# Kernel optimization log

Measured on AMD Instinct MI355X. Metric: run time of the kernel, lower is better.

The kernel has to match this reference:

```python
import jax, jax.numpy as jnp
import numpy as np

N_NODES = 100000
N_EDGES = 1000000
HEADS = 3
NEG_SLOPE_ATTN = 0.2   # DGL EdgeGATConv default negative_slope
NEG_SLOPE_MLP = 0.01   # torch nn.LeakyReLU default


def _edge_softmax(e, dst, num_nodes):
    # softmax over incoming edges of each destination node; e: [E,H]
    m = jax.ops.segment_max(e, dst, num_segments=num_nodes)
    ex = jnp.exp(e - m[dst])
    s = jax.ops.segment_sum(ex, dst, num_segments=num_nodes)
    return ex / s[dst]


def _edge_gat(h, ef, src, dst, Wfc, Wedge, al, ar, ae, Wres, b, D):
    # Faithful to dgl.nn.EdgeGATConv (residual=True, bias=True defaults).
    N = h.shape[0]
    H = HEADS
    ft = (h @ Wfc).reshape(N, H, D)        # [N,H,D] projected node feats
    fe = (ef @ Wedge).reshape(-1, H, D)    # [E,H,D] projected edge feats
    el = jnp.einsum('nhd,hd->nh', ft, al)
    er = jnp.einsum('nhd,hd->nh', ft, ar)
    ee = jnp.einsum('ehd,hd->eh', fe, ae)
    e = jax.nn.leaky_relu(el[src] + er[dst] + ee, NEG_SLOPE_ATTN)  # [E,H]
    a = _edge_softmax(e, dst, N)                                   # [E,H]
    rst = jax.ops.segment_sum(ft[src] * a[..., None], dst, num_segments=N)
    # residual projection + bias (DGL defaults residual=True, bias=True)
    return rst + (h @ Wres).reshape(N, H, D) + b.reshape(1, H, D)


def _forward(node_feats, edge_feats,
             W1, We1, al1, ar1, ae1, Wr1, b1,
             W2, We2, al2, ar2, ae2, Wr2, b2,
             W3, We3, al3, ar3, ae3, Wr3, b3,
             L1a_w, L1a_b, L1b_w, L1b_b, L1c_w, L1c_b, L2_w, L2_b,
             src, dst):
    h1 = _edge_gat(node_feats, edge_feats, src, dst, W1, We1, al1, ar1, ae1, Wr1, b1, 8)
    h2 = _edge_gat(h1.mean(axis=1), edge_feats, src, dst, W2, We2, al2, ar2, ae2, Wr2, b2, 16)
    h3 = _edge_gat(h2.mean(axis=1), edge_feats, src, dst, W3, We3, al3, ar3, ae3, Wr3, b3, 32)
    # linear1 MLP head applied per (node, head)
    x = jax.nn.leaky_relu(h3 @ L1a_w + L1a_b, NEG_SLOPE_MLP)   # [N,H,16]
    x = jax.nn.leaky_relu(x @ L1b_w + L1b_b, NEG_SLOPE_MLP)    # [N,H,4]
    x = x @ L1c_w + L1c_b                                       # [N,H,1]
    x = x.reshape(x.shape[0], -1) @ L2_w + L2_b                 # [N,1]
    return jnp.max(x, axis=0)                                   # [1]


def setup_inputs() -> dict:
    key = jax.random.key(0)
    ks = iter(jax.random.split(key, 64))

    def nrm(shape, scale=0.1):
        return jax.random.normal(next(ks), shape, dtype=jnp.float32) * scale

    inp = {
        'node_feats': jax.random.normal(next(ks), (N_NODES, 6), dtype=jnp.float32),
        'edge_feats': jax.random.uniform(next(ks), (N_EDGES, 1), dtype=jnp.float32),
    }
    dims = [(6, 8), (8, 16), (16, 32)]
    for i, (din, dout) in enumerate(dims, start=1):
        inp[f'W{i}'] = nrm((din, HEADS * dout))
        inp[f'We{i}'] = nrm((1, HEADS * dout))
        inp[f'al{i}'] = nrm((HEADS, dout))
        inp[f'ar{i}'] = nrm((HEADS, dout))
        inp[f'ae{i}'] = nrm((HEADS, dout))
        inp[f'Wr{i}'] = nrm((din, HEADS * dout))
        inp[f'b{i}'] = nrm((HEADS * dout,))
    inp['L1a_w'] = nrm((32, 16)); inp['L1a_b'] = nrm((16,))
    inp['L1b_w'] = nrm((16, 4));  inp['L1b_b'] = nrm((4,))
    inp['L1c_w'] = nrm((4, 1));   inp['L1c_b'] = nrm((1,))
    inp['L2_w'] = nrm((HEADS, 1)); inp['L2_b'] = nrm((1,))
    inp['src'] = jax.random.randint(next(ks), (N_EDGES,), 0, N_NODES, dtype=jnp.int32)
    inp['dst'] = jax.random.randint(next(ks), (N_EDGES,), 0, N_NODES, dtype=jnp.int32)
    return inp


def reference(node_feats, edge_feats,
              W1, We1, al1, ar1, ae1, Wr1, b1,
              W2, We2, al2, ar2, ae2, Wr2, b2,
              W3, We3, al3, ar3, ae3, Wr3, b3,
              L1a_w, L1a_b, L1b_w, L1b_b, L1c_w, L1c_b, L2_w, L2_b,
              src, dst):
    return _forward(node_feats, edge_feats,
                    W1, We1, al1, ar1, ae1, Wr1, b1,
                    W2, We2, al2, ar2, ae2, Wr2, b2,
                    W3, We3, al3, ar3, ae3, Wr3, b3,
                    L1a_w, L1a_b, L1b_w, L1b_b, L1c_w, L1c_b, L2_w, L2_b,
                    src, dst)
```

## Files before the change

### kernel.cpp

```cpp
#include <hip/hip_runtime.h>
#include <hip/hip_fp16.h>
#include <math.h>

#define NN 100000
#define NE 1000000
#define NCHUNK 160
#define CHUNK (NE/NCHUNK)
#define NODE_RANGE (NN/8)
#define CAPS 24
#define GXS (NCHUNK*8)

typedef unsigned int   u32;
typedef unsigned short u16;

__device__ __forceinline__ float lrelu(float x, float sl){ return x >= 0.f ? x : sl*x; }

__device__ __forceinline__ void atomicMaxF(float* a, float v){
    if (v >= 0.f) atomicMax((int*)a, __float_as_int(v));
    else          atomicMin((unsigned int*)a, __float_as_uint(v));
}

template<int DIN, int DINP, int D, bool WRM>
__device__ void coefBody(const float* __restrict__ Wfc, const float* __restrict__ al,
                         const float* __restrict__ ar, const float* __restrict__ We,
                         const float* __restrict__ ae, const float* __restrict__ Wres,
                         const float* __restrict__ bias,
                         float* __restrict__ q, float* __restrict__ r, float* __restrict__ ce,
                         float* __restrict__ wrm, float* __restrict__ bm){
    int t = threadIdx.x;
    for (int i = t; i < 3*DINP; i += 256){
        int hd = i/DINP, k = i - hd*DINP;
        float qa = 0.f, ra = 0.f;
        if (k < DIN){
            for (int d = 0; d < D; ++d){
                float w = Wfc[k*3*D + hd*D + d];
                qa += w*al[hd*D+d];
                ra += w*ar[hd*D+d];
            }
        }
        q[i] = qa; r[i] = ra;
    }
    if (t < 3){
        float c = 0.f;
        for (int d = 0; d < D; ++d) c += We[t*D+d]*ae[t*D+d];
        ce[t] = c;
    }
    if (WRM){
        for (int i = t; i < DIN*D; i += 256){
            int k = i/D, d = i - k*D;
            wrm[i] = (Wres[k*3*D+d] + Wres[k*3*D+D+d] + Wres[k*3*D+2*D+d])*(1.f/3.f);
        }
        for (int i = t; i < D; i += 256)
            bm[i] = (bias[i] + bias[D+i] + bias[2*D+i])*(1.f/3.f);
    }
}

__global__ void __launch_bounds__(256) kScatPrep(
    const int* __restrict__ src, const int* __restrict__ dst,
    const float* __restrict__ ef,
    int* __restrict__ deg, u32* __restrict__ pack,
    int* __restrict__ ovfc, int4* __restrict__ ovf,
    const float* W1, const float* al1, const float* ar1, const float* We1,
    const float* ae1, const float* Wr1, const float* b1,
    const float* W2, const float* al2, const float* ar2, const float* We2,
    const float* ae2, const float* Wr2, const float* b2,
    const float* W3, const float* al3, const float* ar3, const float* We3,
    const float* ae3, const float* Wr3, const float* b3,
    const float* L1a_w, const float* L1a_b,
    float* coef, float* FA, float* FR, float* C0,
    const float* __restrict__ nf, u32* __restrict__ ntab1, float* __restrict__ er3a,
    float* __restrict__ out)
{
    if (blockIdx.x < GXS){
        const int xcd  = blockIdx.x & 7;
        const int base = (blockIdx.x >> 3)*CHUNK;
        for (int e = base + threadIdx.x; e < base + CHUNK; e += 256){
            int d = __builtin_nontemporal_load(dst + e);
            if (d / NODE_RANGE == xcd){
                int s    = __builtin_nontemporal_load(src + e);
                float fv = __builtin_nontemporal_load(ef + e);
                int pos = atomicAdd(&deg[d], 1);
                if (pos < CAPS){
                    u32 rec = ((u32)s << 15) | (u32)(fv*32767.f + 0.5f);
                    pack[(size_t)d*CAPS + pos] = rec;
                } else {
                    int o = atomicAdd(ovfc, 1);
                    ovf[o] = make_int4(d, s, __float_as_int(fv), 0);
                }
            }
        }
        return;
    }
    const int bid = blockIdx.x - GXS;
    if (bid == 0){
        if (threadIdx.x == 255) out[0] = -INFINITY;
        coefBody<6,8,8,true>(W1, al1, ar1, We1, ae1, Wr1, b1,
            coef+0, coef+24, coef+48, coef+52, coef+100);
    } else if (bid == 1){
        coefBody<8,8,16,true>(W2, al2, ar2, We2, ae2, Wr2, b2,
            coef+108, coef+132, coef+156, coef+160, coef+288);
    } else if (bid == 2){
        coefBody<16,16,32,false>(W3, al3, ar3, We3, ae3, Wr3, b3,
            coef+304, coef+352, coef+400, nullptr, nullptr);
    } else if (bid == 3){
        int t = threadIdx.x;
        for (int i = t; i < 768; i += 256){
            int hd = i >> 8, rem = i & 255;
            int k = rem >> 4, ii = rem & 15;
            float a = 0.f, r = 0.f;
            for (int d = 0; d < 32; ++d){
                float w = L1a_w[d*16 + ii];
                a += W3[k*96 + hd*32 + d]*w;
                r += Wr3[k*96 + hd*32 + d]*w;
            }
            FA[i] = a; FR[i] = r;
        }
        if (t < 48){
            int hd = t >> 4, ii = t & 15;
            float c = L1a_b[ii];
            for (int d = 0; d < 32; ++d) c += b3[hd*32 + d]*L1a_w[d*16 + ii];
            C0[t] = c;
        }
    } else {
        __shared__ float r1s[24];
        int t = threadIdx.x;
        if (t < 24){
            int hd = t >> 3, k = t & 7;
            float ra = 0.f;
            if (k < 6)
                for (int d = 0; d < 8; ++d) ra += W1[k*24 + hd*8 + d]*ar1[hd*8 + d];
            r1s[t] = ra;
        }
        __syncthreads();
        int n = (bid - 4)*256 + t;
        if (n >= NN) return;
        float h[6];
        #pragma unroll
        for (int k = 0; k < 6; ++k) h[k] = nf[(size_t)n*6 + k];
        __half2 p0 = __floats2half2_rn(h[0], h[1]);
        __half2 p1 = __floats2half2_rn(h[2], h[3]);
        __half2 p2 = __floats2half2_rn(h[4], h[5]);
        __half2 p3 = __floats2half2_rn(0.f, 0.f);
        uint4 row;
        row.x = *(u32*)&p0; row.y = *(u32*)&p1; row.z = *(u32*)&p2; row.w = *(u32*)&p3;
        *(uint4*)(ntab1 + (size_t)n*4) = row;
        #pragma unroll
        for (int hd = 0; hd < 3; ++hd){
            float er = 0.f;
            #pragma unroll
            for (int k = 0; k < 6; ++k) er += r1s[hd*8+k]*h[k];
            er3a[(size_t)n*3+hd] = er;
        }
    }
}

template<int DINP, int DINR, int D, bool AGG>
__global__ void __launch_bounds__(256) kNode(
    const int* __restrict__ deg, const u32* __restrict__ pack,
    const int* __restrict__ ovfc, const int4* __restrict__ ovf,
    const u32* __restrict__ ntab,
    const float* __restrict__ er3, const float* __restrict__ qc,
    const float* __restrict__ cep, const float* __restrict__ hres,
    const float* __restrict__ Wfc, const float* __restrict__ Wr2,
    const float* __restrict__ b2,
    float* __restrict__ hmean_o, u32* __restrict__ ntab_next,
    float* __restrict__ er3_next, const float* __restrict__ rnext,
    float* __restrict__ agg_o)
{
    constexpr int KS   = DINP/4;
    constexpr int ROWU = DINP/2;
    constexpr int D4   = D/4;
    const int tid  = threadIdx.x;
    const int lid  = tid & 63;
    const int lane = tid & 3;
    const int n    = (blockIdx.x*256 + tid) >> 2;
    const bool alive = n < NN;

    int dg = 0;
    float e0 = 0.f, e1 = 0.f, e2 = 0.f;
    if (alive){
        dg = deg[n]; if (dg > CAPS) dg = CAPS;
        e0 = er3[(size_t)n*3+0]; e1 = er3[(size_t)n*3+1]; e2 = er3[(size_t)n*3+2];
    }
    const float c0 = cep[0], c1 = cep[1], c2 = cep[2];
    float q[3*KS];
    #pragma unroll
    for (int hd = 0; hd < 3; ++hd)
        #pragma unroll
        for (int ks = 0; ks < KS; ++ks)
            q[hd*KS+ks] = qc[hd*DINP + lane*KS + ks];

    float acc[3*KS];
    #pragma unroll
    for (int v = 0; v < 3*KS; ++v) acc[v] = 0.f;
    float s0 = 0.f, s1 = 0.f, s2 = 0.f;

    auto rowLoad = [&](int sv, u32& w0, u32& w1){
        const u32* rp = ntab + (size_t)sv*ROWU + lane*(KS/2);
        if constexpr (KS == 2){ w0 = rp[0]; w1 = 0u; }
        else { uint2 t2 = *(const uint2*)rp; w0 = t2.x; w1 = t2.y; }
    };
    auto edgeCompute = [&](float fv, u32 w0, u32 w1){
        float hv[KS];
        float2 f = __half22float2(*(__half2*)&w0);
        hv[0] = f.x; hv[1] = f.y;
        if constexpr (KS == 4){
            f = __half22float2(*(__half2*)&w1);
            hv[2] = f.x; hv[3] = f.y;
        }
        float l0 = 0.f, l1 = 0.f, l2 = 0.f;
        #pragma unroll
        for (int ks = 0; ks < KS; ++ks){
            l0 += q[ks]*hv[ks]; l1 += q[KS+ks]*hv[ks]; l2 += q[2*KS+ks]*hv[ks];
        }
        l0 += __shfl_xor(l0,1); l0 += __shfl_xor(l0,2);
        l1 += __shfl_xor(l1,1); l1 += __shfl_xor(l1,2);
        l2 += __shfl_xor(l2,1); l2 += __shfl_xor(l2,2);
        float x0 = __expf(lrelu(l0 + e0 + c0*fv, 0.2f));
        float x1 = __expf(lrelu(l1 + e1 + c1*fv, 0.2f));
        float x2 = __expf(lrelu(l2 + e2 + c2*fv, 0.2f));
        s0 += x0; s1 += x1; s2 += x2;
        #pragma unroll
        for (int ks = 0; ks < KS; ++ks){
            acc[ks]      += x0*hv[ks];
            acc[KS+ks]   += x1*hv[ks];
            acc[2*KS+ks] += x2*hv[ks];
        }
    };

    int p = n*CAPS;
    const int re = p + dg;
    while (p + 1 < re){
        u32 ra = pack[p], rb = pack[p+1];
        u32 a0, a1, b0, b1;
        rowLoad((int)(ra >> 15), a0, a1);
        rowLoad((int)(rb >> 15), b0, b1);
        edgeCompute((float)(ra & 0x7fffu)*(1.f/32767.f), a0, a1);
        edgeCompute((float)(rb & 0x7fffu)*(1.f/32767.f), b0, b1);
        p += 2;
    }
    if (p < re){
        u32 ra = pack[p];
        u32 a0, a1;
        rowLoad((int)(ra >> 15), a0, a1);
        edgeCompute((float)(ra & 0x7fffu)*(1.f/32767.f), a0, a1);
    }

    int nov = ovfc[0];
    for (int i = 0; i < nov; ++i){
        int4 o = ovf[i];
        if (alive && o.x == n){
            u32 a0, a1;
            rowLoad(o.y, a0, a1);
            edgeCompute(__int_as_float(o.z), a0, a1);
        }
    }

    float i0 = s0 > 0.f ? 1.f/s0 : 0.f;
    float i1 = s1 > 0.f ? 1.f/s1 : 0.f;
    float i2 = s2 > 0.f ? 1.f/s2 : 0.f;
    if constexpr (!AGG){ i0 *= (1.f/3.f); i1 *= (1.f/3.f); i2 *= (1.f/3.f); }
    #pragma unroll
    for (int ks = 0; ks < KS; ++ks){
        acc[ks] *= i0; acc[KS+ks] *= i1; acc[2*KS+ks] *= i2;
    }

    if constexpr (AGG){
        if (alive){
            #pragma unroll
            for (int hd = 0; hd < 3; ++hd){
                float4 v = make_float4(acc[hd*KS+0], acc[hd*KS+1], acc[hd*KS+2], acc[hd*KS+3]);
                *(float4*)(agg_o + (size_t)n*48 + hd*16 + lane*4) = v;
            }
        }
        return;
    } else {
        float hsl[KS];
        #pragma unroll
        for (int ks = 0; ks < KS; ++ks){
            int k = lane*KS + ks;
            hsl[ks] = (alive && k < DINR) ? hres[(size_t)n*DINR + k] : 0.f;
        }
        float hm[D4];
        #pragma unroll
        for (int i = 0; i < D4; ++i) hm[i] = b2[lane*D4 + i];
        #pragma unroll
        for (int r = 0; r < 4; ++r){
            int sl = (lid & ~3) | ((lid + r) & 3);
            int kb = ((lane + r) & 3)*KS;
            float as[3*KS], hs[KS];
            #pragma unroll
            for (int v = 0; v < 3*KS; ++v) as[v] = __shfl(acc[v], sl);
            #pragma unroll
            for (int v = 0; v < KS; ++v) hs[v] = __shfl(hsl[v], sl);
            #pragma unroll
            for (int ks = 0; ks < KS; ++ks){
                int k = kb + ks;
                if (DINP == DINR || k < DINR){
                    #pragma unroll
                    for (int i = 0; i < D4; ++i){
                        int d = lane*D4 + i;
                        hm[i] += as[ks]     *Wfc[k*3*D + d]
                               + as[KS+ks]  *Wfc[k*3*D + D + d]
                               + as[2*KS+ks]*Wfc[k*3*D + 2*D + d]
                               + hs[ks]     *Wr2[k*D + d];
                    }
                }
            }
        }
        if (alive){
            #pragma unroll
            for (int i = 0; i < D4; ++i)
                hmean_o[(size_t)n*D + lane*D4 + i] = hm[i];
            #pragma unroll
            for (int w = 0; w < D4/2; ++w){
                __half2 hh = __floats2half2_rn(hm[2*w], hm[2*w+1]);
                ntab_next[(size_t)n*(D/2) + lane*(D4/2) + w] = *(u32*)&hh;
            }
        }
        float p0 = 0.f, p1 = 0.f, p2 = 0.f;
        #pragma unroll
        for (int i = 0; i < D4; ++i){
            int d = lane*D4 + i;
            p0 += rnext[0*D + d]*hm[i];
            p1 += rnext[1*D + d]*hm[i];
            p2 += rnext[2*D + d]*hm[i];
        }
        p0 += __shfl_xor(p0,1); p0 += __shfl_xor(p0,2);
        p1 += __shfl_xor(p1,1); p1 += __shfl_xor(p1,2);
        p2 += __shfl_xor(p2,1); p2 += __shfl_xor(p2,2);
        if (alive && lane < 3){
            float v = (lane == 0) ? p0 : ((lane == 1) ? p1 : p2);
            er3_next[(size_t)n*3 + lane] = v;
        }
    }
}

__global__ void __launch_bounds__(256) kFin3(
    const float* __restrict__ agg,
    const float* __restrict__ hres,
    const float* __restrict__ FAg, const float* __restrict__ FRg,
    const float* __restrict__ C0g,
    const float* __restrict__ L1b_w, const float* __restrict__ L1b_b,
    const float* __restrict__ L1c_w, const float* __restrict__ L1c_b,
    const float* __restrict__ L2_w, const float* __restrict__ L2_b,
    float* __restrict__ out)
{
    const int tid = threadIdx.x;
    const int n = blockIdx.x*256 + tid;
    float y = -INFINITY;
    if (n < NN){
        float hr[16];
        const float4* hr4 = (const float4*)(hres + (size_t)n*16);
        #pragma unroll
        for (int w = 0; w < 4; ++w){
            float4 v = hr4[w];
            hr[4*w]=v.x; hr[4*w+1]=v.y; hr[4*w+2]=v.z; hr[4*w+3]=v.w;
        }
        float acc = L2_b[0];
        for (int hd = 0; hd < 3; ++hd){
            float ag[16];
            const float4* ag4 = (const float4*)(agg + (size_t)n*48 + hd*16);
            #pragma unroll
            for (int w = 0; w < 4; ++w){
                float4 v = ag4[w];
                ag[4*w]=v.x; ag[4*w+1]=v.y; ag[4*w+2]=v.z; ag[4*w+3]=v.w;
            }
            float x1[16];
            #pragma unroll
            for (int i = 0; i < 16; ++i) x1[i] = C0g[hd*16 + i];
            #pragma unroll
            for (int k = 0; k < 16; ++k){
                const float a = ag[k], h = hr[k];
                const float* fap = FAg + hd*256 + k*16;
                const float* frp = FRg + hd*256 + k*16;
                #pragma unroll
                for (int i = 0; i < 16; ++i)
                    x1[i] += a*fap[i] + h*frp[i];
            }
            #pragma unroll
            for (int i = 0; i < 16; ++i) x1[i] = lrelu(x1[i], 0.01f);
            float x2[4];
            #pragma unroll
            for (int ii = 0; ii < 4; ++ii){
                float a = L1b_b[ii];
                #pragma unroll
                for (int i = 0; i < 16; ++i) a += x1[i]*L1b_w[i*4+ii];
                x2[ii] = lrelu(a, 0.01f);
            }
            float v = L1c_b[0];
            #pragma unroll
            for (int ii = 0; ii < 4; ++ii) v += x2[ii]*L1c_w[ii];
            acc += v*L2_w[hd];
        }
        y = acc;
    }
    __shared__ float red[256];
    red[tid] = y;
    __syncthreads();
    for (int o = 128; o > 0; o >>= 1){
        if (tid < o) red[tid] = fmaxf(red[tid], red[tid+o]);
        __syncthreads();
    }
    if (tid == 0) atomicMaxF(out, red[0]);
}

extern "C" void kernel_launch(void* const* d_in, const int* in_sizes, int n_in,
                              void* d_out, int out_size, void* d_ws, size_t ws_size,
                              hipStream_t stream) {
    const float* nf  = (const float*)d_in[0];
    const float* ef  = (const float*)d_in[1];
    const float* W1  = (const float*)d_in[2];
    const float* We1 = (const float*)d_in[3];
    const float* al1 = (const float*)d_in[4];
    const float* ar1 = (const float*)d_in[5];
    const float* ae1 = (const float*)d_in[6];
    const float* Wr1 = (const float*)d_in[7];
    const float* b1  = (const float*)d_in[8];
    const float* W2  = (const float*)d_in[9];
    const float* We2 = (const float*)d_in[10];
    const float* al2 = (const float*)d_in[11];
    const float* ar2 = (const float*)d_in[12];
    const float* ae2 = (const float*)d_in[13];
    const float* Wr2 = (const float*)d_in[14];
    const float* b2  = (const float*)d_in[15];
    const float* W3  = (const float*)d_in[16];
    const float* We3 = (const float*)d_in[17];
    const float* al3 = (const float*)d_in[18];
    const float* ar3 = (const float*)d_in[19];
    const float* ae3 = (const float*)d_in[20];
    const float* Wr3 = (const float*)d_in[21];
    const float* b3  = (const float*)d_in[22];
    const float* L1a_w = (const float*)d_in[23];
    const float* L1a_b = (const float*)d_in[24];
    const float* L1b_w = (const float*)d_in[25];
    const float* L1b_b = (const float*)d_in[26];
    const float* L1c_w = (const float*)d_in[27];
    const float* L1c_b = (const float*)d_in[28];
    const float* L2_w  = (const float*)d_in[29];
    const float* L2_b  = (const float*)d_in[30];
    const int* src = (const int*)d_in[31];
    const int* dst = (const int*)d_in[32];
    float* out = (float*)d_out;

    float* ws = (float*)d_ws;
    u32* ntab1 = (u32*)ws;
    u32* ntab2 = ntab1 + (size_t)NN*4;
    u32* ntab3 = ntab2 + (size_t)NN*4;
    float* f   = (float*)(ntab3 + (size_t)NN*8);
    float* hm2  = f;  f += (size_t)NN*8;
    float* hm3  = f;  f += (size_t)NN*16;
    float* aggb = f;  f += (size_t)NN*48;
    float* er3a = f;  f += (size_t)NN*3;
    float* er3b = f;  f += (size_t)NN*3;
    float* coef = f;  f += 512;
    float* FAb = f;  f += 768;
    float* FRb = f;  f += 768;
    float* C0b = f;  f += 64;
    int* deg  = (int*)f;
    int* ovfc = deg + NN;
    int4* ovf = (int4*)(ovfc + 4);
    u32* pack = (u32*)(ovf + 4096);

    const int gSP = GXS + 4 + (NN + 255)/256;
    const int gN  = (NN + 255)/256;
    const int gT  = (NN*4 + 255)/256;

    hipMemsetAsync(deg, 0, (NN + 4)*sizeof(int), stream);

    kScatPrep<<<gSP,256,0,stream>>>(src, dst, ef, deg, pack, ovfc, ovf,
                                    W1, al1, ar1, We1, ae1, Wr1, b1,
                                    W2, al2, ar2, We2, ae2, Wr2, b2,
                                    W3, al3, ar3, We3, ae3, Wr3, b3,
                                    L1a_w, L1a_b, coef, FAb, FRb, C0b,
                                    nf, ntab1, er3a, out);

    kNode<8,6,8,false><<<gT,256,0,stream>>>(deg, pack, ovfc, ovf, ntab1, er3a,
        coef+0, coef+48, nf, W1, coef+52, coef+100,
        hm2, ntab2, er3b, coef+132, nullptr);

    kNode<8,8,16,false><<<gT,256,0,stream>>>(deg, pack, ovfc, ovf, ntab2, er3b,
        coef+108, coef+156, hm2, W2, coef+160, coef+288,
        hm3, ntab3, er3a, coef+352, nullptr);

    kNode<16,16,32,true><<<gT,256,0,stream>>>(deg, pack, ovfc, ovf, ntab3, er3a,
        coef+304, coef+400, hm3, W3, nullptr, nullptr,
        nullptr, nullptr, nullptr, nullptr, aggb);

    kFin3<<<gN,256,0,stream>>>(aggb, hm3, FAb, FRb, C0b,
        L1b_w, L1b_b, L1c_w, L1c_b, L2_w, L2_b, out);
}
```

Before: 173.9 us.

## Fuse MLP head into last node kernel and vectorize edge scatter loads

```diff
diff --git a/kernel.cpp b/kernel.cpp
--- a/kernel.cpp
+++ b/kernel.cpp
@@ -12,6 +12,7 @@
 
 typedef unsigned int   u32;
 typedef unsigned short u16;
+typedef long long      s64;
 
 __device__ __forceinline__ float lrelu(float x, float sl){ return x >= 0.f ? x : sl*x; }
 
@@ -74,19 +75,27 @@
     if (blockIdx.x < GXS){
         const int xcd  = blockIdx.x & 7;
         const int base = (blockIdx.x >> 3)*CHUNK;
-        for (int e = base + threadIdx.x; e < base + CHUNK; e += 256){
-            int d = __builtin_nontemporal_load(dst + e);
-            if (d / NODE_RANGE == xcd){
-                int s    = __builtin_nontemporal_load(src + e);
-                float fv = __builtin_nontemporal_load(ef + e);
-                int pos = atomicAdd(&deg[d], 1);
-                if (pos < CAPS){
-                    u32 rec = ((u32)s << 15) | (u32)(fv*32767.f + 0.5f);
-                    pack[(size_t)d*CAPS + pos] = rec;
-                } else {
-                    int o = atomicAdd(ovfc, 1);
-                    ovf[o] = make_int4(d, s, __float_as_int(fv), 0);
-                }
+        for (int e = base + threadIdx.x*2; e < base + CHUNK; e += 512){
+            s64 dp = __builtin_nontemporal_load((const s64*)(dst + e));
+            int d0 = (int)dp, d1 = (int)(dp >> 32);
+            bool m0 = (d0/NODE_RANGE == xcd), m1 = (d1/NODE_RANGE == xcd);
+            if (!(m0|m1)) continue;
+            s64 sp = __builtin_nontemporal_load((const s64*)(src + e));
+            float f0 = __builtin_nontemporal_load(ef + e);
+            float f1 = __builtin_nontemporal_load(ef + e + 1);
+            int s0 = (int)sp, s1 = (int)(sp >> 32);
+            int pos0 = -1, pos1 = -1;
+            if (m0) pos0 = atomicAdd(&deg[d0], 1);
+            if (m1) pos1 = atomicAdd(&deg[d1], 1);
+            if (m0){
+                if (pos0 < CAPS)
+                    pack[(size_t)d0*CAPS + pos0] = ((u32)s0 << 15) | (u32)(f0*32767.f + 0.5f);
+                else { int o = atomicAdd(ovfc, 1); ovf[o] = make_int4(d0, s0, __float_as_int(f0), 0); }
+            }
+            if (m1){
+                if (pos1 < CAPS)
+                    pack[(size_t)d1*CAPS + pos1] = ((u32)s1 << 15) | (u32)(f1*32767.f + 0.5f);
+                else { int o = atomicAdd(ovfc, 1); ovf[o] = make_int4(d1, s1, __float_as_int(f1), 0); }
             }
         }
         return;
@@ -165,7 +174,12 @@
     const float* __restrict__ b2,
     float* __restrict__ hmean_o, u32* __restrict__ ntab_next,
     float* __restrict__ er3_next, const float* __restrict__ rnext,
-    float* __restrict__ agg_o)
+    const float* __restrict__ FAg, const float* __restrict__ FRg,
+    const float* __restrict__ C0g,
+    const float* __restrict__ L1b_w, const float* __restrict__ L1b_b,
+    const float* __restrict__ L1c_w, const float* __restrict__ L1c_b,
+    const float* __restrict__ L2_w, const float* __restrict__ L2_b,
+    float* __restrict__ out)
 {
     constexpr int KS   = DINP/4;
     constexpr int ROWU = DINP/2;
@@ -266,13 +280,59 @@
     }
 
     if constexpr (AGG){
-        if (alive){
-            #pragma unroll
-            for (int hd = 0; hd < 3; ++hd){
-                float4 v = make_float4(acc[hd*KS+0], acc[hd*KS+1], acc[hd*KS+2], acc[hd*KS+3]);
-                *(float4*)(agg_o + (size_t)n*48 + hd*16 + lane*4) = v;
-            }
-        }
+        float hrl[KS];
+        #pragma unroll
+        for (int ks = 0; ks < KS; ++ks)
+            hrl[ks] = alive ? hres[(size_t)n*DINR + lane*KS + ks] : 0.f;
+        float y = 0.f;
+        #pragma unroll
+        for (int hd = 0; hd < 3; ++hd){
+            float x1[16];
+            #pragma unroll
+            for (int i = 0; i < 16; ++i) x1[i] = 0.f;
+            #pragma unroll
+            for (int ks = 0; ks < KS; ++ks){
+                const float a = acc[hd*KS+ks];
+                const float h = hrl[ks];
+                const float4* fap = (const float4*)(FAg + hd*256 + (lane*KS+ks)*16);
+                const float4* frp = (const float4*)(FRg + hd*256 + (lane*KS+ks)*16);
+                #pragma unroll
+                for (int w = 0; w < 4; ++w){
+                    float4 fa4 = fap[w], fr4 = frp[w];
+                    x1[4*w+0] += a*fa4.x + h*fr4.x;
+                    x1[4*w+1] += a*fa4.y + h*fr4.y;
+                    x1[4*w+2] += a*fa4.z + h*fr4.z;
+                    x1[4*w+3] += a*fa4.w + h*fr4.w;
+                }
+            }
+            #pragma unroll
+            for (int i = 0; i < 16; ++i){
+                x1[i] += __shfl_xor(x1[i], 1);
+                x1[i] += __shfl_xor(x1[i], 2);
+                x1[i] = lrelu(x1[i] + C0g[hd*16 + i], 0.01f);
+            }
+            float x2[4];
+            #pragma unroll
+            for (int ii = 0; ii < 4; ++ii){
+                float a = L1b_b[ii];
+                #pragma unroll
+                for (int i = 0; i < 16; ++i) a += x1[i]*L1b_w[i*4+ii];
+                x2[ii] = lrelu(a, 0.01f);
+            }
+            float v = L1c_b[0];
+            #pragma unroll
+            for (int ii = 0; ii < 4; ++ii) v += x2[ii]*L1c_w[ii];
+            y += v*L2_w[hd];
+        }
+        float ymax = alive ? (y + L2_b[0]) : -INFINITY;
+        __shared__ float red[256];
+        red[tid] = ymax;
+        __syncthreads();
+        for (int o = 128; o > 0; o >>= 1){
+            if (tid < o) red[tid] = fmaxf(red[tid], red[tid+o]);
+            __syncthreads();
+        }
+        if (tid == 0) atomicMaxF(out, red[0]);
         return;
     } else {
         float hsl[KS];
@@ -334,75 +394,6 @@
             er3_next[(size_t)n*3 + lane] = v;
         }
     }
-}
-
-__global__ void __launch_bounds__(256) kFin3(
-    const float* __restrict__ agg,
-    const float* __restrict__ hres,
-    const float* __restrict__ FAg, const float* __restrict__ FRg,
-    const float* __restrict__ C0g,
-    const float* __restrict__ L1b_w, const float* __restrict__ L1b_b,
-    const float* __restrict__ L1c_w, const float* __restrict__ L1c_b,
-    const float* __restrict__ L2_w, const float* __restrict__ L2_b,
-    float* __restrict__ out)
-{
-    const int tid = threadIdx.x;
-    const int n = blockIdx.x*256 + tid;
-    float y = -INFINITY;
-    if (n < NN){
-        float hr[16];
-        const float4* hr4 = (const float4*)(hres + (size_t)n*16);
-        #pragma unroll
-        for (int w = 0; w < 4; ++w){
-            float4 v = hr4[w];
-            hr[4*w]=v.x; hr[4*w+1]=v.y; hr[4*w+2]=v.z; hr[4*w+3]=v.w;
-        }
-        float acc = L2_b[0];
-        for (int hd = 0; hd < 3; ++hd){
-            float ag[16];
-            const float4* ag4 = (const float4*)(agg + (size_t)n*48 + hd*16);
-            #pragma unroll
-            for (int w = 0; w < 4; ++w){
-                float4 v = ag4[w];
-                ag[4*w]=v.x; ag[4*w+1]=v.y; ag[4*w+2]=v.z; ag[4*w+3]=v.w;
-            }
-            float x1[16];
-            #pragma unroll
-            for (int i = 0; i < 16; ++i) x1[i] = C0g[hd*16 + i];
-            #pragma unroll
-            for (int k = 0; k < 16; ++k){
-                const float a = ag[k], h = hr[k];
-                const float* fap = FAg + hd*256 + k*16;
-                const float* frp = FRg + hd*256 + k*16;
-                #pragma unroll
-                for (int i = 0; i < 16; ++i)
-                    x1[i] += a*fap[i] + h*frp[i];
-            }
-            #pragma unroll
-            for (int i = 0; i < 16; ++i) x1[i] = lrelu(x1[i], 0.01f);
-            float x2[4];
-            #pragma unroll
-            for (int ii = 0; ii < 4; ++ii){
-                float a = L1b_b[ii];
-                #pragma unroll
-                for (int i = 0; i < 16; ++i) a += x1[i]*L1b_w[i*4+ii];
-                x2[ii] = lrelu(a, 0.01f);
-            }
-            float v = L1c_b[0];
-            #pragma unroll
-            for (int ii = 0; ii < 4; ++ii) v += x2[ii]*L1c_w[ii];
-            acc += v*L2_w[hd];
-        }
-        y = acc;
-    }
-    __shared__ float red[256];
-    red[tid] = y;
-    __syncthreads();
-    for (int o = 128; o > 0; o >>= 1){
-        if (tid < o) red[tid] = fmaxf(red[tid], red[tid+o]);
-        __syncthreads();
-    }
-    if (tid == 0) atomicMaxF(out, red[0]);
 }
 
 extern "C" void kernel_launch(void* const* d_in, const int* in_sizes, int n_in,
@@ -450,7 +441,6 @@
     float* f   = (float*)(ntab3 + (size_t)NN*8);
     float* hm2  = f;  f += (size_t)NN*8;
     float* hm3  = f;  f += (size_t)NN*16;
-    float* aggb = f;  f += (size_t)NN*48;
     float* er3a = f;  f += (size_t)NN*3;
     float* er3b = f;  f += (size_t)NN*3;
     float* coef = f;  f += 512;
@@ -463,7 +453,6 @@
     u32* pack = (u32*)(ovf + 4096);
 
     const int gSP = GXS + 4 + (NN + 255)/256;
-    const int gN  = (NN + 255)/256;
     const int gT  = (NN*4 + 255)/256;
 
     hipMemsetAsync(deg, 0, (NN + 4)*sizeof(int), stream);
@@ -477,16 +466,16 @@
 
     kNode<8,6,8,false><<<gT,256,0,stream>>>(deg, pack, ovfc, ovf, ntab1, er3a,
         coef+0, coef+48, nf, W1, coef+52, coef+100,
-        hm2, ntab2, er3b, coef+132, nullptr);
+        hm2, ntab2, er3b, coef+132,
+        nullptr,nullptr,nullptr,nullptr,nullptr,nullptr,nullptr,nullptr,nullptr, nullptr);
 
     kNode<8,8,16,false><<<gT,256,0,stream>>>(deg, pack, ovfc, ovf, ntab2, er3b,
         coef+108, coef+156, hm2, W2, coef+160, coef+288,
-        hm3, ntab3, er3a, coef+352, nullptr);
+        hm3, ntab3, er3a, coef+352,
+        nullptr,nullptr,nullptr,nullptr,nullptr,nullptr,nullptr,nullptr,nullptr, nullptr);
 
     kNode<16,16,32,true><<<gT,256,0,stream>>>(deg, pack, ovfc, ovf, ntab3, er3a,
-        coef+304, coef+400, hm3, W3, nullptr, nullptr,
-        nullptr, nullptr, nullptr, nullptr, aggb);
-
-    kFin3<<<gN,256,0,stream>>>(aggb, hm3, FAb, FRb, C0b,
-        L1b_w, L1b_b, L1c_w, L1c_b, L2_w, L2_b, out);
+        coef+304, coef+400, hm3, nullptr, nullptr, nullptr,
+        nullptr, nullptr, nullptr, nullptr,
+        FAb, FRb, C0b, L1b_w, L1b_b, L1c_w, L1c_b, L2_w, L2_b, out);
 }
```

New measurement: 272.7 us. 1.57x slower.
